# Kernel tuning notes

Hardware: AMD Instinct MI355X
Metric: run time of the kernel (lower is better)

Reference implementation:

```python
import jax, jax.numpy as jnp
import numpy as np

B, S, H, D = 2, 2048, 32, 128


def setup_inputs() -> dict:
    key = jax.random.key(0)
    qkv = jax.random.normal(key, (B, S, 3, H, D), dtype=jnp.float32)
    return {"qkv": qkv, "causal": 1}


def reference(qkv, causal):
    # qkv: [B, S, 3, H, D] packed as in flash_attn qkvpacked convention.
    # Distributed all-to-all / ring rotation is identity math on one device,
    # so this is standard scaled-dot-product attention.
    q = qkv[:, :, 0]  # [B, S, H, D]
    k = qkv[:, :, 1]
    v = qkv[:, :, 2]
    scale = 1.0 / jnp.sqrt(jnp.asarray(q.shape[-1], q.dtype))
    # [B, H, S, S]
    logits = jnp.einsum("bshd,bthd->bhst", q, k) * scale
    if causal:
        s = q.shape[1]
        mask = jnp.tril(jnp.ones((s, s), dtype=bool))  # [S, S]
        logits = jnp.where(mask[None, None], logits, jnp.finfo(logits.dtype).min)
    probs = jax.nn.softmax(logits, axis=-1)
    out = jnp.einsum("bhst,bthd->bshd", probs, v)  # [B, S, H, D]
    return out
```

## Files before the change

### kernel.cpp

```cpp
#include <hip/hip_runtime.h>
#include <hip/hip_bf16.h>

constexpr int Bc = 2;
constexpr int Sc = 2048;
constexpr int Hc = 32;
constexpr int Dc = 128;
constexpr int QKV_STRIDE = 3 * Hc * Dc;

constexpr int BQ = 128;
constexpr int BK = 64;
constexpr float SCALE_LOG2E = 0.088388347648318f * 1.442695040888963f;
constexpr float DEFER_THR = 8.0f;

constexpr int KST = 132;
constexpr int VST = 68;

typedef __attribute__((ext_vector_type(8)))  short    bf16x8;
typedef __attribute__((ext_vector_type(4)))  short    bf16x4;
typedef __attribute__((ext_vector_type(16))) float    f32x16;
typedef __attribute__((ext_vector_type(4)))  unsigned u32x4;

static __device__ __forceinline__ short f2bf(float f) {
    __bf16 h = (__bf16)f;
    return __builtin_bit_cast(short, h);
}
static __device__ __forceinline__ unsigned pk2(float lo, float hi) {
    union { short2 s; unsigned u; } x;
    x.s.x = f2bf(lo); x.s.y = f2bf(hi);
    return x.u;
}
static __device__ __forceinline__ void lds_barrier() {
    asm volatile("s_waitcnt lgkmcnt(0)" ::: "memory");
    __builtin_amdgcn_s_barrier();
    asm volatile("" ::: "memory");
}

__global__ __launch_bounds__(256)
void attn_fwd(const float* __restrict__ qkv,
              const int* __restrict__ causal_p,
              float* __restrict__ out)
{
    const int bid = blockIdx.x;
    const int o   = bid >> 6;
    const int bh  = bid & 63;
    const int r_  = o & 3;
    const int j_  = o >> 2;
    const int bq_ = 15 - 2 * r_;
    const int qt  = (j_ < 2) ? (bq_ - j_) : (15 - bq_ + 3 - j_);

    const int b = bh >> 5;
    const int h = bh & 31;
    const int causal = *causal_p;

    const int tid  = threadIdx.x;
    const int w    = tid >> 6;
    const int lane = tid & 63;
    const int l31  = lane & 31;
    const int hf   = lane >> 5;

    __shared__ short Ks[64 * KST];
    __shared__ short Vs[128 * VST];

    const int q0  = qt * BQ;
    const int wq0 = q0 + w * 32;

    const int kg = tid >> 5;
    const int dl = tid & 31;

    const float* kplane = qkv + (size_t)b * Sc * QKV_STRIDE + Hc * Dc + h * Dc;

    bf16x8 qf[8];
    {
        const float* qb = qkv + (size_t)(b * Sc + wq0 + l31) * QKV_STRIDE + h * Dc;
        #pragma unroll
        for (int st = 0; st < 8; ++st) {
            const float* p = qb + st * 16 + hf * 8;
            float4 x0 = *(const float4*)(p);
            float4 x1 = *(const float4*)(p + 4);
            bf16x8 q;
            q[0] = f2bf(x0.x * SCALE_LOG2E);
            q[1] = f2bf(x0.y * SCALE_LOG2E);
            q[2] = f2bf(x0.z * SCALE_LOG2E);
            q[3] = f2bf(x0.w * SCALE_LOG2E);
            q[4] = f2bf(x1.x * SCALE_LOG2E);
            q[5] = f2bf(x1.y * SCALE_LOG2E);
            q[6] = f2bf(x1.z * SCALE_LOG2E);
            q[7] = f2bf(x1.w * SCALE_LOG2E);
            qf[st] = q;
        }
    }

    f32x16 o_[4];
    #pragma unroll
    for (int db = 0; db < 4; ++db)
        #pragma unroll
        for (int i = 0; i < 16; ++i) o_[db][i] = 0.f;
    float m = -1e30f, l = 0.f;

    const int nkv = causal ? (2 * qt + 2) : (Sc / BK);

    float4 kst[8];
    float  vst[8][4];

    auto issue = [&](int kt) {
        const float* kb = kplane + (size_t)(kt * BK + kg * 8) * QKV_STRIDE;
        #pragma unroll
        for (int j = 0; j < 8; ++j)
            kst[j] = *(const float4*)(kb + (size_t)j * QKV_STRIDE + dl * 4);
        const float* vb = kb + Hc * Dc;
        #pragma unroll
        for (int j = 0; j < 8; ++j) {
            #pragma unroll
            for (int q = 0; q < 4; ++q)
                vst[j][q] = vb[(size_t)j * QKV_STRIDE + q * 32 + dl];
        }
    };

    auto commit = [&]() {
        #pragma unroll
        for (int j = 0; j < 8; ++j) {
            bf16x4 kk;
            kk[0] = f2bf(kst[j].x); kk[1] = f2bf(kst[j].y);
            kk[2] = f2bf(kst[j].z); kk[3] = f2bf(kst[j].w);
            *(bf16x4*)&Ks[(kg * 8 + j) * KST + dl * 4] = kk;
        }
        #pragma unroll
        for (int q = 0; q < 4; ++q) {
            bf16x8 vv;
            #pragma unroll
            for (int j = 0; j < 8; ++j) vv[j] = f2bf(vst[j][q]);
            *(bf16x8*)&Vs[(q * 32 + dl) * VST + kg * 8] = vv;
        }
    };

    issue(0);

    for (int kt = 0; kt < nkv; ++kt) {
        lds_barrier();
        commit();
        if (kt + 1 < nkv) issue(kt + 1);
        lds_barrier();

        const int kbase = kt * BK;
        if (causal && kbase > wq0 + 31) continue;

        f32x16 acc[2];
        #pragma unroll
        for (int mb = 0; mb < 2; ++mb)
            #pragma unroll
            for (int i = 0; i < 16; ++i) acc[mb][i] = 0.f;
        __builtin_amdgcn_s_setprio(1);
        #pragma unroll
        for (int st = 0; st < 8; ++st) {
            #pragma unroll
            for (int mb = 0; mb < 2; ++mb) {
                bf16x8 ka = *(const bf16x8*)&Ks[(mb * 32 + l31) * KST + st * 16 + hf * 8];
                acc[mb] = __builtin_amdgcn_mfma_f32_32x32x16_bf16(ka, qf[st], acc[mb], 0, 0, 0);
            }
        }
        __builtin_amdgcn_s_setprio(0);

        if (causal && kbase + 63 > wq0) {
            const int qg = wq0 + l31;
            #pragma unroll
            for (int mb = 0; mb < 2; ++mb) {
                #pragma unroll
                for (int r = 0; r < 16; ++r) {
                    const int kgl = kbase + mb * 32 + (r & 3) + 8 * (r >> 2) + 4 * hf;
                    if (kgl > qg) acc[mb][r] = -1e30f;
                }
            }
        }

        float pm = acc[0][0];
        #pragma unroll
        for (int i = 1; i < 16; ++i) pm = fmaxf(pm, acc[0][i]);
        #pragma unroll
        for (int i = 0; i < 16; ++i) pm = fmaxf(pm, acc[1][i]);
        pm = fmaxf(pm, __shfl_xor(pm, 32));
        if (__any(pm > m + DEFER_THR)) {
            const float mnew  = fmaxf(m, pm);
            const float alpha = __builtin_amdgcn_exp2f(m - mnew);
            m = mnew; l *= alpha;
            #pragma unroll
            for (int r = 0; r < 16; ++r) {
                const float ar = __shfl(alpha, (r & 3) + 8 * (r >> 2) + 4 * hf);
                o_[0][r] *= ar; o_[1][r] *= ar; o_[2][r] *= ar; o_[3][r] *= ar;
            }
        }
        float rs = 0.f;
        #pragma unroll
        for (int i = 0; i < 16; ++i) {
            const float p = __builtin_amdgcn_exp2f(acc[0][i] - m);
            acc[0][i] = p; rs += p;
        }
        #pragma unroll
        for (int i = 0; i < 16; ++i) {
            const float p = __builtin_amdgcn_exp2f(acc[1][i] - m);
            acc[1][i] = p; rs += p;
        }
        rs += __shfl_xor(rs, 32);
        l += rs;

        unsigned wpk[2][4][2];
        #pragma unroll
        for (int mb = 0; mb < 2; ++mb)
            #pragma unroll
            for (int c = 0; c < 4; ++c) {
                wpk[mb][c][0] = pk2(acc[mb][4 * c + 0], acc[mb][4 * c + 1]);
                wpk[mb][c][1] = pk2(acc[mb][4 * c + 2], acc[mb][4 * c + 3]);
            }
        unsigned cross[2][2][2];
        #pragma unroll
        for (int mb = 0; mb < 2; ++mb)
            #pragma unroll
            for (int ci = 0; ci < 2; ++ci)
                #pragma unroll
                for (int wd = 0; wd < 2; ++wd) {
                    const unsigned send = hf ? wpk[mb][2 * ci][wd] : wpk[mb][2 * ci + 1][wd];
                    cross[mb][ci][wd] = (unsigned)__shfl_xor((int)send, 32);
                }
        bf16x8 pa[4];
        #pragma unroll
        for (int ks = 0; ks < 4; ++ks) {
            const int mb = ks >> 1, ci = ks & 1;
            u32x4 wv;
            wv[0] = hf ? cross[mb][ci][0] : wpk[mb][2 * ci][0];
            wv[1] = hf ? cross[mb][ci][1] : wpk[mb][2 * ci][1];
            wv[2] = hf ? wpk[mb][2 * ci + 1][0] : cross[mb][ci][0];
            wv[3] = hf ? wpk[mb][2 * ci + 1][1] : cross[mb][ci][1];
            pa[ks] = __builtin_bit_cast(bf16x8, wv);
        }

        __builtin_amdgcn_s_setprio(1);
        #pragma unroll
        for (int ks = 0; ks < 4; ++ks) {
            #pragma unroll
            for (int db = 0; db < 4; ++db) {
                bf16x8 vb = *(const bf16x8*)&Vs[(db * 32 + l31) * VST + ks * 16 + hf * 8];
                o_[db] = __builtin_amdgcn_mfma_f32_32x32x16_bf16(pa[ks], vb, o_[db], 0, 0, 0);
            }
        }
        __builtin_amdgcn_s_setprio(0);
    }

    #pragma unroll
    for (int r = 0; r < 16; ++r) {
        const int rq = (r & 3) + 8 * (r >> 2) + 4 * hf;
        const float lr = __shfl(l, rq);
        const float inv = 1.f / lr;
        const int qg = wq0 + rq;
        float* ob = out + (size_t)(b * Sc + qg) * (Hc * Dc) + h * Dc + l31;
        ob[0]  = o_[0][r] * inv;
        ob[32] = o_[1][r] * inv;
        ob[64] = o_[2][r] * inv;
        ob[96] = o_[3][r] * inv;
    }
}

extern "C" void kernel_launch(void* const* d_in, const int* in_sizes, int n_in,
                              void* d_out, int out_size, void* d_ws, size_t ws_size,
                              hipStream_t stream) {
    const float* qkv = (const float*)d_in[0];
    const int* causal = (const int*)d_in[1];
    float* out = (float*)d_out;
    dim3 grid((Sc / BQ) * Bc * Hc);
    attn_fwd<<<grid, 256, 0, stream>>>(qkv, causal, out);
}
```

Baseline: 200.6 us.

## Double-buffer K/V LDS tiles with smaller 32-key blocks and one barrier per step

Halves the key block to 32 and adds a second LDS buffer for K and V. The next tile is committed and prefetched while the current one is computed, so each step needs one barrier instead of two. This is meant to cut barrier stalls and overlap global loads with MFMA work, and the finer block also trims masked work on the causal diagonal. The cost is twice as many loop iterations, each with more softmax and shuffle overhead relative to its MFMA work, and fewer MFMAs per iteration to hide latency.

Result: slower. 266.8 us (+33.0%).

```diff
diff --git a/kernel.cpp b/kernel.cpp
--- a/kernel.cpp
+++ b/kernel.cpp
@@ -8,12 +8,12 @@
 constexpr int QKV_STRIDE = 3 * Hc * Dc;
 
 constexpr int BQ = 128;
-constexpr int BK = 64;
+constexpr int BK = 32;
 constexpr float SCALE_LOG2E = 0.088388347648318f * 1.442695040888963f;
 constexpr float DEFER_THR = 8.0f;
 
 constexpr int KST = 132;
-constexpr int VST = 68;
+constexpr int VST = 36;
 
 typedef __attribute__((ext_vector_type(8)))  short    bf16x8;
 typedef __attribute__((ext_vector_type(4)))  short    bf16x4;
@@ -58,8 +58,8 @@
     const int l31  = lane & 31;
     const int hf   = lane >> 5;
 
-    __shared__ short Ks[64 * KST];
-    __shared__ short Vs[128 * VST];
+    __shared__ short Ks[2][BK * KST];
+    __shared__ short Vs[2][128 * VST];
 
     const int q0  = qt * BQ;
     const int wq0 = q0 + w * 32;
@@ -97,151 +97,137 @@
         for (int i = 0; i < 16; ++i) o_[db][i] = 0.f;
     float m = -1e30f, l = 0.f;
 
-    const int nkv = causal ? (2 * qt + 2) : (Sc / BK);
-
-    float4 kst[8];
-    float  vst[8][4];
+    const int nkv = causal ? (4 * qt + 4) : (Sc / BK);
+
+    float4 kst[4];
+    float  vst[4][4];
 
     auto issue = [&](int kt) {
-        const float* kb = kplane + (size_t)(kt * BK + kg * 8) * QKV_STRIDE;
-        #pragma unroll
-        for (int j = 0; j < 8; ++j)
+        const float* kb = kplane + (size_t)(kt * BK + kg * 4) * QKV_STRIDE;
+        #pragma unroll
+        for (int j = 0; j < 4; ++j)
             kst[j] = *(const float4*)(kb + (size_t)j * QKV_STRIDE + dl * 4);
         const float* vb = kb + Hc * Dc;
         #pragma unroll
-        for (int j = 0; j < 8; ++j) {
+        for (int j = 0; j < 4; ++j) {
             #pragma unroll
             for (int q = 0; q < 4; ++q)
                 vst[j][q] = vb[(size_t)j * QKV_STRIDE + q * 32 + dl];
         }
     };
 
-    auto commit = [&]() {
-        #pragma unroll
-        for (int j = 0; j < 8; ++j) {
+    auto commit = [&](int buf) {
+        #pragma unroll
+        for (int j = 0; j < 4; ++j) {
             bf16x4 kk;
             kk[0] = f2bf(kst[j].x); kk[1] = f2bf(kst[j].y);
             kk[2] = f2bf(kst[j].z); kk[3] = f2bf(kst[j].w);
-            *(bf16x4*)&Ks[(kg * 8 + j) * KST + dl * 4] = kk;
+            *(bf16x4*)&Ks[buf][(kg * 4 + j) * KST + dl * 4] = kk;
         }
         #pragma unroll
         for (int q = 0; q < 4; ++q) {
-            bf16x8 vv;
-            #pragma unroll
-            for (int j = 0; j < 8; ++j) vv[j] = f2bf(vst[j][q]);
-            *(bf16x8*)&Vs[(q * 32 + dl) * VST + kg * 8] = vv;
+            bf16x4 vv;
+            #pragma unroll
+            for (int j = 0; j < 4; ++j) vv[j] = f2bf(vst[j][q]);
+            *(bf16x4*)&Vs[buf][(q * 32 + dl) * VST + kg * 4] = vv;
         }
     };
 
     issue(0);
+    commit(0);
+    issue(1);
+    lds_barrier();
 
     for (int kt = 0; kt < nkv; ++kt) {
+        const int cur = kt & 1;
+        if (kt + 1 < nkv) {
+            commit(cur ^ 1);
+            if (kt + 2 < nkv) issue(kt + 2);
+        }
+
+        const int kbase = kt * BK;
+        if (!(causal && kbase > wq0 + 31)) {
+            f32x16 acc;
+            #pragma unroll
+            for (int i = 0; i < 16; ++i) acc[i] = 0.f;
+            __builtin_amdgcn_s_setprio(1);
+            #pragma unroll
+            for (int st = 0; st < 8; ++st) {
+                bf16x8 ka = *(const bf16x8*)&Ks[cur][l31 * KST + st * 16 + hf * 8];
+                acc = __builtin_amdgcn_mfma_f32_32x32x16_bf16(ka, qf[st], acc, 0, 0, 0);
+            }
+            __builtin_amdgcn_s_setprio(0);
+
+            if (causal && kbase + BK - 1 > wq0) {
+                const int qg = wq0 + l31;
+                #pragma unroll
+                for (int r = 0; r < 16; ++r) {
+                    const int kgl = kbase + (r & 3) + 8 * (r >> 2) + 4 * hf;
+                    if (kgl > qg) acc[r] = -1e30f;
+                }
+            }
+
+            float pm = fmaxf(acc[0], acc[1]);
+            #pragma unroll
+            for (int i = 2; i < 16; ++i) pm = fmaxf(pm, acc[i]);
+            pm = fmaxf(pm, __shfl_xor(pm, 32));
+            if (__any(pm > m + DEFER_THR)) {
+                const float mnew  = fmaxf(m, pm);
+                const float alpha = __builtin_amdgcn_exp2f(m - mnew);
+                m = mnew; l *= alpha;
+                #pragma unroll
+                for (int r = 0; r < 16; ++r) {
+                    const float ar = __shfl(alpha, (r & 3) + 8 * (r >> 2) + 4 * hf);
+                    o_[0][r] *= ar; o_[1][r] *= ar; o_[2][r] *= ar; o_[3][r] *= ar;
+                }
+            }
+            float rs = 0.f;
+            #pragma unroll
+            for (int i = 0; i < 16; ++i) {
+                const float p = __builtin_amdgcn_exp2f(acc[i] - m);
+                acc[i] = p; rs += p;
+            }
+            rs += __shfl_xor(rs, 32);
+            l += rs;
+
+            unsigned wpk[4][2];
+            #pragma unroll
+            for (int c = 0; c < 4; ++c) {
+                wpk[c][0] = pk2(acc[4 * c + 0], acc[4 * c + 1]);
+                wpk[c][1] = pk2(acc[4 * c + 2], acc[4 * c + 3]);
+            }
+            unsigned cross[2][2];
+            #pragma unroll
+            for (int ci = 0; ci < 2; ++ci)
+                #pragma unroll
+                for (int wd = 0; wd < 2; ++wd) {
+                    const unsigned send = hf ? wpk[2 * ci][wd] : wpk[2 * ci + 1][wd];
+                    cross[ci][wd] = (unsigned)__shfl_xor((int)send, 32);
+                }
+            bf16x8 pa[2];
+            #pragma unroll
+            for (int ks = 0; ks < 2; ++ks) {
+                u32x4 wv;
+                wv[0] = hf ? cross[ks][0] : wpk[2 * ks][0];
+                wv[1] = hf ? cross[ks][1] : wpk[2 * ks][1];
+                wv[2] = hf ? wpk[2 * ks + 1][0] : cross[ks][0];
+                wv[3] = hf ? wpk[2 * ks + 1][1] : cross[ks][1];
+                pa[ks] = __builtin_bit_cast(bf16x8, wv);
+            }
+
+            __builtin_amdgcn_s_setprio(1);
+            #pragma unroll
+            for (int ks = 0; ks < 2; ++ks) {
+                #pragma unroll
+                for (int db = 0; db < 4; ++db) {
+                    bf16x8 vb = *(const bf16x8*)&Vs[cur][(db * 32 + l31) * VST + ks * 16 + hf * 8];
+                    o_[db] = __builtin_amdgcn_mfma_f32_32x32x16_bf16(pa[ks], vb, o_[db], 0, 0, 0);
+                }
+            }
+            __builtin_amdgcn_s_setprio(0);
+        }
+
         lds_barrier();
-        commit();
-        if (kt + 1 < nkv) issue(kt + 1);
-        lds_barrier();
-
-        const int kbase = kt * BK;
-        if (causal && kbase > wq0 + 31) continue;
-
-        f32x16 acc[2];
-        #pragma unroll
-        for (int mb = 0; mb < 2; ++mb)
-            #pragma unroll
-            for (int i = 0; i < 16; ++i) acc[mb][i] = 0.f;
-        __builtin_amdgcn_s_setprio(1);
-        #pragma unroll
-        for (int st = 0; st < 8; ++st) {
-            #pragma unroll
-            for (int mb = 0; mb < 2; ++mb) {
-                bf16x8 ka = *(const bf16x8*)&Ks[(mb * 32 + l31) * KST + st * 16 + hf * 8];
-                acc[mb] = __builtin_amdgcn_mfma_f32_32x32x16_bf16(ka, qf[st], acc[mb], 0, 0, 0);
-            }
-        }
-        __builtin_amdgcn_s_setprio(0);
-
-        if (causal && kbase + 63 > wq0) {
-            const int qg = wq0 + l31;
-            #pragma unroll
-            for (int mb = 0; mb < 2; ++mb) {
-                #pragma unroll
-                for (int r = 0; r < 16; ++r) {
-                    const int kgl = kbase + mb * 32 + (r & 3) + 8 * (r >> 2) + 4 * hf;
-                    if (kgl > qg) acc[mb][r] = -1e30f;
-                }
-            }
-        }
-
-        float pm = acc[0][0];
-        #pragma unroll
-        for (int i = 1; i < 16; ++i) pm = fmaxf(pm, acc[0][i]);
-        #pragma unroll
-        for (int i = 0; i < 16; ++i) pm = fmaxf(pm, acc[1][i]);
-        pm = fmaxf(pm, __shfl_xor(pm, 32));
-        if (__any(pm > m + DEFER_THR)) {
-            const float mnew  = fmaxf(m, pm);
-            const float alpha = __builtin_amdgcn_exp2f(m - mnew);
-            m = mnew; l *= alpha;
-            #pragma unroll
-            for (int r = 0; r < 16; ++r) {
-                const float ar = __shfl(alpha, (r & 3) + 8 * (r >> 2) + 4 * hf);
-                o_[0][r] *= ar; o_[1][r] *= ar; o_[2][r] *= ar; o_[3][r] *= ar;
-            }
-        }
-        float rs = 0.f;
-        #pragma unroll
-        for (int i = 0; i < 16; ++i) {
-            const float p = __builtin_amdgcn_exp2f(acc[0][i] - m);
-            acc[0][i] = p; rs += p;
-        }
-        #pragma unroll
-        for (int i = 0; i < 16; ++i) {
-            const float p = __builtin_amdgcn_exp2f(acc[1][i] - m);
-            acc[1][i] = p; rs += p;
-        }
-        rs += __shfl_xor(rs, 32);
-        l += rs;
-
-        unsigned wpk[2][4][2];
-        #pragma unroll
-        for (int mb = 0; mb < 2; ++mb)
-            #pragma unroll
-            for (int c = 0; c < 4; ++c) {
-                wpk[mb][c][0] = pk2(acc[mb][4 * c + 0], acc[mb][4 * c + 1]);
-                wpk[mb][c][1] = pk2(acc[mb][4 * c + 2], acc[mb][4 * c + 3]);
-            }
-        unsigned cross[2][2][2];
-        #pragma unroll
-        for (int mb = 0; mb < 2; ++mb)
-            #pragma unroll
-            for (int ci = 0; ci < 2; ++ci)
-                #pragma unroll
-                for (int wd = 0; wd < 2; ++wd) {
-                    const unsigned send = hf ? wpk[mb][2 * ci][wd] : wpk[mb][2 * ci + 1][wd];
-                    cross[mb][ci][wd] = (unsigned)__shfl_xor((int)send, 32);
-                }
-        bf16x8 pa[4];
-        #pragma unroll
-        for (int ks = 0; ks < 4; ++ks) {
-            const int mb = ks >> 1, ci = ks & 1;
-            u32x4 wv;
-            wv[0] = hf ? cross[mb][ci][0] : wpk[mb][2 * ci][0];
-            wv[1] = hf ? cross[mb][ci][1] : wpk[mb][2 * ci][1];
-            wv[2] = hf ? wpk[mb][2 * ci + 1][0] : cross[mb][ci][0];
-            wv[3] = hf ? wpk[mb][2 * ci + 1][1] : cross[mb][ci][1];
-            pa[ks] = __builtin_bit_cast(bf16x8, wv);
-        }
-
-        __builtin_amdgcn_s_setprio(1);
-        #pragma unroll
-        for (int ks = 0; ks < 4; ++ks) {
-            #pragma unroll
-            for (int db = 0; db < 4; ++db) {
-                bf16x8 vb = *(const bf16x8*)&Vs[(db * 32 + l31) * VST + ks * 16 + hf * 8];
-                o_[db] = __builtin_amdgcn_mfma_f32_32x32x16_bf16(pa[ks], vb, o_[db], 0, 0, 0);
-            }
-        }
-        __builtin_amdgcn_s_setprio(0);
     }
 
     #pragma unroll
```
